# Optimization experiments

Measured on AMD Instinct MI355X. Metric: run time of the kernel, lower is better.

The kernel has to match this reference:

```python
import jax, jax.numpy as jnp
import numpy as np


def setup_inputs() -> dict:
    key = jax.random.key(0)
    ks = jax.random.split(key, 6)
    N, E, D = 50000, 400000, 128
    x = jax.random.normal(ks[0], (N, D), dtype=jnp.float32)
    edge_attr = jax.random.normal(ks[1], (E, D), dtype=jnp.float32)
    edge_index = jax.random.randint(ks[2], (2, E), 0, N, dtype=jnp.int64)
    # LatentMLP: two linear layers (3*D -> D -> D) with ReLU activations
    W1 = jax.random.normal(ks[3], (3 * D, D), dtype=jnp.float32) * (1.0 / np.sqrt(3 * D))
    b1 = jnp.zeros((D,), dtype=jnp.float32)
    W2 = jax.random.normal(ks[4], (D, D), dtype=jnp.float32) * (1.0 / np.sqrt(D))
    b2 = jnp.zeros((D,), dtype=jnp.float32)
    return {"x": x, "edge_attr": edge_attr, "edge_index": edge_index,
            "W1": W1, "b1": b1, "W2": W2, "b2": b2}


def reference(x, edge_attr, edge_index, W1, b1, W2, b2):
    src, dst = edge_index[0], edge_index[1]
    # gather node features per edge: [E, D] each
    agg = jnp.concatenate([x[src], x[dst], edge_attr], axis=1)  # [E, 3D]
    h = jax.nn.relu(agg @ W1 + b1)   # [E, D]
    out = jax.nn.relu(h @ W2 + b2)   # [E, D] -> new edge_attr
    return out
```

## Files before the change

kernel.cpp:

```cpp
#include <hip/hip_runtime.h>
#include <hip/hip_bf16.h>

typedef __bf16 bf16_t;
typedef __bf16 bf16x8 __attribute__((ext_vector_type(8)));
typedef __bf16 bf16x4 __attribute__((ext_vector_type(4)));
typedef float  f32x4  __attribute__((ext_vector_type(4)));

#define D  128
#define BM 128

__device__ __forceinline__ int swz(int r, int c) {
    return (r * D + c) ^ ((r & 7) << 3);
}

__global__ void prep_weights_kernel(const float* __restrict__ W1,
                                    const float* __restrict__ W2,
                                    bf16_t* __restrict__ ws) {
    int t = blockIdx.x * 256 + threadIdx.x;
    int s = t >> 14, r = t & 16383;
    int n = r >> 7, k = r & 127;
    float v = (s < 3) ? W1[(s * 128 + k) * 128 + n] : W2[k * 128 + n];
    ws[t] = (bf16_t)v;
}

__global__ __launch_bounds__(256, 2)
void fused_edge_mlp_kernel(const float* __restrict__ x,
                           const float* __restrict__ ea,
                           const int* __restrict__ ei,
                           const bf16_t* __restrict__ ws,
                           const float* __restrict__ b1,
                           const float* __restrict__ b2,
                           float* __restrict__ out,
                           int E) {
    __shared__ __align__(16) bf16_t Ab[BM * D];
    __shared__ __align__(16) bf16_t Bb[D * D];

    const int tid  = threadIdx.x;
    const int lane = tid & 63;
    const int wv   = tid >> 6;
    const int col0 = lane & 15;
    const int krow = lane >> 4;
    const int l31  = lane & 31;
    const int half = lane >> 5;
    const int e0   = blockIdx.x * BM;

    const int erL  = min(e0 + wv * 32 + l31, E - 1);
    const int sidx = ei[erL];
    const int didx = ei[E + erL];

    const int brow_t = tid >> 4;
    const int bslot  = (tid & 15) * 8;

    f32x4  abuf[16];
    bf16x8 bnext[8];

    {
        const bf16_t* base = ws;
#pragma unroll
        for (int j = 0; j < 8; j++)
            bnext[j] = *(const bf16x8*)(base + (j * 16 + brow_t) * 128 + bslot);
    }
#pragma unroll
    for (int j = 0; j < 16; j++) {
        int r = j * 2 + half;
        int g = __shfl(sidx, r);
        abuf[j] = *(const f32x4*)(x + (long long)g * D + l31 * 4);
    }

    float bias1[8], bias2[8];
#pragma unroll
    for (int n = 0; n < 8; n++) { bias1[n] = b1[n*16 + col0]; bias2[n] = b2[n*16 + col0]; }

#pragma unroll
    for (int j = 0; j < 8; j++)
        *(bf16x8*)&Bb[swz(j * 16 + brow_t, bslot)] = bnext[j];
#pragma unroll
    for (int j = 0; j < 16; j++) {
        int r = j * 2 + half;
        f32x4 v = abuf[j];
        bf16x4 hv = { (bf16_t)v.x, (bf16_t)v.y, (bf16_t)v.z, (bf16_t)v.w };
        *(bf16x4*)&Ab[swz(wv * 32 + r, l31 * 4)] = hv;
    }
    __syncthreads();

    f32x4 acc[2][8];
#pragma unroll
    for (int m = 0; m < 2; m++)
#pragma unroll
        for (int n = 0; n < 8; n++) acc[m][n] = (f32x4){0.f, 0.f, 0.f, 0.f};

#pragma unroll
    for (int p = 0; p < 4; p++) {
        if (p < 3) {
            const bf16_t* base = ws + (p + 1) * 16384;
#pragma unroll
            for (int j = 0; j < 8; j++)
                bnext[j] = *(const bf16x8*)(base + (j * 16 + brow_t) * 128 + bslot);
        }
        if (p < 2) {
#pragma unroll
            for (int j = 0; j < 16; j++) {
                int r = j * 2 + half;
                const float* rp;
                if (p == 0) { int g = __shfl(didx, r); rp = x + (long long)g * D; }
                else        { int e = min(e0 + wv * 32 + r, E - 1); rp = ea + (long long)e * D; }
                abuf[j] = *(const f32x4*)(rp + l31 * 4);
            }
        }

#pragma unroll
        for (int kk = 0; kk < 4; kk++) {
            bf16x8 a0 = *(const bf16x8*)&Ab[swz(wv*32 +      col0, kk*32 + krow*8)];
            bf16x8 a1 = *(const bf16x8*)&Ab[swz(wv*32 + 16 + col0, kk*32 + krow*8)];
#pragma unroll
            for (int n = 0; n < 8; n++) {
                bf16x8 b = *(const bf16x8*)&Bb[swz(n*16 + col0, kk*32 + krow*8)];
                acc[0][n] = __builtin_amdgcn_mfma_f32_16x16x32_bf16(a0, b, acc[0][n], 0, 0, 0);
                acc[1][n] = __builtin_amdgcn_mfma_f32_16x16x32_bf16(a1, b, acc[1][n], 0, 0, 0);
            }
        }

        if (p < 2) {
#pragma unroll
            for (int j = 0; j < 16; j++) {
                int r = j * 2 + half;
                f32x4 v = abuf[j];
                bf16x4 hv = { (bf16_t)v.x, (bf16_t)v.y, (bf16_t)v.z, (bf16_t)v.w };
                *(bf16x4*)&Ab[swz(wv * 32 + r, l31 * 4)] = hv;
            }
        }
        if (p == 2) {
#pragma unroll
            for (int m = 0; m < 2; m++)
#pragma unroll
                for (int n = 0; n < 8; n++)
#pragma unroll
                    for (int ri = 0; ri < 4; ri++) {
                        float hv = fmaxf(acc[m][n][ri] + bias1[n], 0.f);
                        Ab[swz(wv*32 + m*16 + krow*4 + ri, n*16 + col0)] = (bf16_t)hv;
                    }
#pragma unroll
            for (int m = 0; m < 2; m++)
#pragma unroll
                for (int n = 0; n < 8; n++) acc[m][n] = (f32x4){0.f, 0.f, 0.f, 0.f};
        }
        if (p < 3) {
            __syncthreads();
#pragma unroll
            for (int j = 0; j < 8; j++)
                *(bf16x8*)&Bb[swz(j * 16 + brow_t, bslot)] = bnext[j];
            __syncthreads();
        }
    }

#pragma unroll
    for (int m = 0; m < 2; m++)
#pragma unroll
        for (int n = 0; n < 8; n++)
#pragma unroll
            for (int ri = 0; ri < 4; ri++) {
                int row = wv*32 + m*16 + krow*4 + ri;
                int e = e0 + row;
                if (e < E) out[(long long)e * D + n*16 + col0] = fmaxf(acc[m][n][ri] + bias2[n], 0.f);
            }
}

extern "C" void kernel_launch(void* const* d_in, const int* in_sizes, int n_in,
                              void* d_out, int out_size, void* d_ws, size_t ws_size,
                              hipStream_t stream) {
    const float* x  = (const float*)d_in[0];
    const float* ea = (const float*)d_in[1];
    const int*   ei = (const int*)d_in[2];
    const float* W1 = (const float*)d_in[3];
    const float* b1 = (const float*)d_in[4];
    const float* W2 = (const float*)d_in[5];
    const float* b2 = (const float*)d_in[6];
    float* out = (float*)d_out;

    const int E = in_sizes[1] / D;

    bf16_t* wsl = (bf16_t*)d_ws;

    prep_weights_kernel<<<256, 256, 0, stream>>>(W1, W2, wsl);

    int nblocks = (E + BM - 1) / BM;
    fused_edge_mlp_kernel<<<nblocks, 256, 0, stream>>>(x, ea, ei, wsl, b1, b2, out, E);
}
```

Before: 144.2 us.

## Read pre-swizzled MFMA weight fragments from global instead of staging in LDS

The weight prep kernel now writes W1 and W2 in the exact per-lane bf16x8 fragment order that the MFMA B operand expects. The main kernel loads B fragments straight from global memory (served by L1/L2) rather than staging each 128x128 weight slice in shared memory. This drops the 32KB B buffer and every block-wide __syncthreads, and raises the launch-bounds occupancy hint from 2 to 3 blocks per CU. In exchange, each wave re-reads the full weight set through the cache hierarchy with no register prefetch, which adds L2 traffic and exposes load latency right before the MFMAs in a kernel that is already bandwidth-heavy.

```diff
diff --git a/kernel.cpp b/kernel.cpp
--- a/kernel.cpp
+++ b/kernel.cpp
@@ -17,13 +17,21 @@
                                     const float* __restrict__ W2,
                                     bf16_t* __restrict__ ws) {
     int t = blockIdx.x * 256 + threadIdx.x;
-    int s = t >> 14, r = t & 16383;
-    int n = r >> 7, k = r & 127;
-    float v = (s < 3) ? W1[(s * 128 + k) * 128 + n] : W2[k * 128 + n];
-    ws[t] = (bf16_t)v;
+    int lane = t & 63, g = t >> 6;
+    int n = g & 7, kk = (g >> 3) & 3, s = g >> 5;
+    int row = n * 16 + (lane & 15);
+    int k0 = kk * 32 + (lane >> 4) * 8;
+    bf16x8 v;
+#pragma unroll
+    for (int j = 0; j < 8; j++) {
+        int k = k0 + j;
+        float f = (s < 3) ? W1[(s * 128 + k) * 128 + row] : W2[k * 128 + row];
+        v[j] = (bf16_t)f;
+    }
+    *(bf16x8*)(ws + t * 8) = v;
 }
 
-__global__ __launch_bounds__(256, 2)
+__global__ __launch_bounds__(256, 3)
 void fused_edge_mlp_kernel(const float* __restrict__ x,
                            const float* __restrict__ ea,
                            const int* __restrict__ ei,
@@ -33,7 +41,6 @@
                            float* __restrict__ out,
                            int E) {
     __shared__ __align__(16) bf16_t Ab[BM * D];
-    __shared__ __align__(16) bf16_t Bb[D * D];
 
     const int tid  = threadIdx.x;
     const int lane = tid & 63;
@@ -48,32 +55,17 @@
     const int sidx = ei[erL];
     const int didx = ei[E + erL];
 
-    const int brow_t = tid >> 4;
-    const int bslot  = (tid & 15) * 8;
+    f32x4 abuf[16];
 
-    f32x4  abuf[16];
-    bf16x8 bnext[8];
-
-    {
-        const bf16_t* base = ws;
-#pragma unroll
-        for (int j = 0; j < 8; j++)
-            bnext[j] = *(const bf16x8*)(base + (j * 16 + brow_t) * 128 + bslot);
-    }
 #pragma unroll
     for (int j = 0; j < 16; j++) {
         int r = j * 2 + half;
         int g = __shfl(sidx, r);
         abuf[j] = *(const f32x4*)(x + (long long)g * D + l31 * 4);
     }
-
     float bias1[8], bias2[8];
 #pragma unroll
     for (int n = 0; n < 8; n++) { bias1[n] = b1[n*16 + col0]; bias2[n] = b2[n*16 + col0]; }
-
-#pragma unroll
-    for (int j = 0; j < 8; j++)
-        *(bf16x8*)&Bb[swz(j * 16 + brow_t, bslot)] = bnext[j];
 #pragma unroll
     for (int j = 0; j < 16; j++) {
         int r = j * 2 + half;
@@ -81,7 +73,6 @@
         bf16x4 hv = { (bf16_t)v.x, (bf16_t)v.y, (bf16_t)v.z, (bf16_t)v.w };
         *(bf16x4*)&Ab[swz(wv * 32 + r, l31 * 4)] = hv;
     }
-    __syncthreads();
 
     f32x4 acc[2][8];
 #pragma unroll
@@ -91,12 +82,6 @@
 
 #pragma unroll
     for (int p = 0; p < 4; p++) {
-        if (p < 3) {
-            const bf16_t* base = ws + (p + 1) * 16384;
-#pragma unroll
-            for (int j = 0; j < 8; j++)
-                bnext[j] = *(const bf16x8*)(base + (j * 16 + brow_t) * 128 + bslot);
-        }
         if (p < 2) {
 #pragma unroll
             for (int j = 0; j < 16; j++) {
@@ -112,9 +97,10 @@
         for (int kk = 0; kk < 4; kk++) {
             bf16x8 a0 = *(const bf16x8*)&Ab[swz(wv*32 +      col0, kk*32 + krow*8)];
             bf16x8 a1 = *(const bf16x8*)&Ab[swz(wv*32 + 16 + col0, kk*32 + krow*8)];
+            const bf16_t* bbase = ws + ((p * 4 + kk) * 8 * 64 + lane) * 8;
 #pragma unroll
             for (int n = 0; n < 8; n++) {
-                bf16x8 b = *(const bf16x8*)&Bb[swz(n*16 + col0, kk*32 + krow*8)];
+                bf16x8 b = *(const bf16x8*)(bbase + n * 512);
                 acc[0][n] = __builtin_amdgcn_mfma_f32_16x16x32_bf16(a0, b, acc[0][n], 0, 0, 0);
                 acc[1][n] = __builtin_amdgcn_mfma_f32_16x16x32_bf16(a1, b, acc[1][n], 0, 0, 0);
             }
@@ -143,13 +129,6 @@
             for (int m = 0; m < 2; m++)
 #pragma unroll
                 for (int n = 0; n < 8; n++) acc[m][n] = (f32x4){0.f, 0.f, 0.f, 0.f};
-        }
-        if (p < 3) {
-            __syncthreads();
-#pragma unroll
-            for (int j = 0; j < 8; j++)
-                *(bf16x8*)&Bb[swz(j * 16 + brow_t, bslot)] = bnext[j];
-            __syncthreads();
         }
     }
 
@@ -181,7 +160,7 @@
 
     bf16_t* wsl = (bf16_t*)d_ws;
 
-    prep_weights_kernel<<<256, 256, 0, stream>>>(W1, W2, wsl);
+    prep_weights_kernel<<<32, 256, 0, stream>>>(W1, W2, wsl);
 
     int nblocks = (E + BM - 1) / BM;
     fused_edge_mlp_kernel<<<nblocks, 256, 0, stream>>>(x, ea, ei, wsl, b1, b2, out, E);
```

Measured after the change: 190.9 us. 1.32x slower.

## Load gathered A operands directly into MFMA registers and halve edge tile

Applied to the files above, without the earlier changes.

Each lane now loads its gathered x/edge_attr rows straight from global memory in the MFMA A-fragment layout, converts them to bf16 in registers, and skips the LDS staging of the A tile. Only the hidden activation h goes through shared memory. The edge tile shrinks from 128 to 64 rows, each wave holds one 16-row fragment, and launch bounds go to 3 blocks per CU, aiming to cut LDS traffic and raise occupancy. In exchange, each B tile loaded into LDS is reused by half as many rows, so there are more blocks, more weight reloads per edge and more syncs per edge. Global loads are also less coalesced, each lane reading 32-byte pieces of rows.

```diff
diff --git a/kernel.cpp b/kernel.cpp
--- a/kernel.cpp
+++ b/kernel.cpp
@@ -3,11 +3,10 @@
 
 typedef __bf16 bf16_t;
 typedef __bf16 bf16x8 __attribute__((ext_vector_type(8)));
-typedef __bf16 bf16x4 __attribute__((ext_vector_type(4)));
 typedef float  f32x4  __attribute__((ext_vector_type(4)));
 
 #define D  128
-#define BM 128
+#define BM 64
 
 __device__ __forceinline__ int swz(int r, int c) {
     return (r * D + c) ^ ((r & 7) << 3);
@@ -23,7 +22,7 @@
     ws[t] = (bf16_t)v;
 }
 
-__global__ __launch_bounds__(256, 2)
+__global__ __launch_bounds__(256, 3)
 void fused_edge_mlp_kernel(const float* __restrict__ x,
                            const float* __restrict__ ea,
                            const int* __restrict__ ei,
@@ -32,26 +31,24 @@
                            const float* __restrict__ b2,
                            float* __restrict__ out,
                            int E) {
-    __shared__ __align__(16) bf16_t Ab[BM * D];
     __shared__ __align__(16) bf16_t Bb[D * D];
+    __shared__ __align__(16) bf16_t Hb[BM * D];
 
     const int tid  = threadIdx.x;
     const int lane = tid & 63;
     const int wv   = tid >> 6;
     const int col0 = lane & 15;
     const int krow = lane >> 4;
-    const int l31  = lane & 31;
-    const int half = lane >> 5;
     const int e0   = blockIdx.x * BM;
 
-    const int erL  = min(e0 + wv * 32 + l31, E - 1);
+    const int erL  = min(e0 + wv * 16 + col0, E - 1);
     const int sidx = ei[erL];
     const int didx = ei[E + erL];
 
     const int brow_t = tid >> 4;
     const int bslot  = (tid & 15) * 8;
 
-    f32x4  abuf[16];
+    f32x4  afA[8];
     bf16x8 bnext[8];
 
     {
@@ -60,13 +57,14 @@
         for (int j = 0; j < 8; j++)
             bnext[j] = *(const bf16x8*)(base + (j * 16 + brow_t) * 128 + bslot);
     }
+    {
+        const float* rp = x + (long long)sidx * D + krow * 8;
 #pragma unroll
-    for (int j = 0; j < 16; j++) {
-        int r = j * 2 + half;
-        int g = __shfl(sidx, r);
-        abuf[j] = *(const f32x4*)(x + (long long)g * D + l31 * 4);
+        for (int kk = 0; kk < 4; kk++) {
+            afA[kk*2]   = *(const f32x4*)(rp + kk*32);
+            afA[kk*2+1] = *(const f32x4*)(rp + kk*32 + 4);
+        }
     }
-
     float bias1[8], bias2[8];
 #pragma unroll
     for (int n = 0; n < 8; n++) { bias1[n] = b1[n*16 + col0]; bias2[n] = b2[n*16 + col0]; }
@@ -74,20 +72,12 @@
 #pragma unroll
     for (int j = 0; j < 8; j++)
         *(bf16x8*)&Bb[swz(j * 16 + brow_t, bslot)] = bnext[j];
+
+    f32x4 acc[8];
 #pragma unroll
-    for (int j = 0; j < 16; j++) {
-        int r = j * 2 + half;
-        f32x4 v = abuf[j];
-        bf16x4 hv = { (bf16_t)v.x, (bf16_t)v.y, (bf16_t)v.z, (bf16_t)v.w };
-        *(bf16x4*)&Ab[swz(wv * 32 + r, l31 * 4)] = hv;
-    }
+    for (int n = 0; n < 8; n++) acc[n] = (f32x4){0.f, 0.f, 0.f, 0.f};
+
     __syncthreads();
-
-    f32x4 acc[2][8];
-#pragma unroll
-    for (int m = 0; m < 2; m++)
-#pragma unroll
-        for (int n = 0; n < 8; n++) acc[m][n] = (f32x4){0.f, 0.f, 0.f, 0.f};
 
 #pragma unroll
     for (int p = 0; p < 4; p++) {
@@ -97,53 +87,50 @@
             for (int j = 0; j < 8; j++)
                 bnext[j] = *(const bf16x8*)(base + (j * 16 + brow_t) * 128 + bslot);
         }
+
+        bf16x8 a_cur[4];
+        if (p < 3) {
+#pragma unroll
+            for (int kk = 0; kk < 4; kk++) {
+                f32x4 lo = afA[kk*2], hi = afA[kk*2+1];
+                a_cur[kk] = (bf16x8){ (bf16_t)lo.x,(bf16_t)lo.y,(bf16_t)lo.z,(bf16_t)lo.w,
+                                      (bf16_t)hi.x,(bf16_t)hi.y,(bf16_t)hi.z,(bf16_t)hi.w };
+            }
+        }
         if (p < 2) {
+            const float* rp = (p == 0) ? (x + (long long)didx * D + krow * 8)
+                                       : (ea + (long long)erL * D + krow * 8);
 #pragma unroll
-            for (int j = 0; j < 16; j++) {
-                int r = j * 2 + half;
-                const float* rp;
-                if (p == 0) { int g = __shfl(didx, r); rp = x + (long long)g * D; }
-                else        { int e = min(e0 + wv * 32 + r, E - 1); rp = ea + (long long)e * D; }
-                abuf[j] = *(const f32x4*)(rp + l31 * 4);
+            for (int kk = 0; kk < 4; kk++) {
+                afA[kk*2]   = *(const f32x4*)(rp + kk*32);
+                afA[kk*2+1] = *(const f32x4*)(rp + kk*32 + 4);
             }
         }
 
 #pragma unroll
         for (int kk = 0; kk < 4; kk++) {
-            bf16x8 a0 = *(const bf16x8*)&Ab[swz(wv*32 +      col0, kk*32 + krow*8)];
-            bf16x8 a1 = *(const bf16x8*)&Ab[swz(wv*32 + 16 + col0, kk*32 + krow*8)];
+            bf16x8 a;
+            if (p < 3) a = a_cur[kk];
+            else       a = *(const bf16x8*)&Hb[swz(wv*16 + col0, kk*32 + krow*8)];
 #pragma unroll
             for (int n = 0; n < 8; n++) {
                 bf16x8 b = *(const bf16x8*)&Bb[swz(n*16 + col0, kk*32 + krow*8)];
-                acc[0][n] = __builtin_amdgcn_mfma_f32_16x16x32_bf16(a0, b, acc[0][n], 0, 0, 0);
-                acc[1][n] = __builtin_amdgcn_mfma_f32_16x16x32_bf16(a1, b, acc[1][n], 0, 0, 0);
+                acc[n] = __builtin_amdgcn_mfma_f32_16x16x32_bf16(a, b, acc[n], 0, 0, 0);
             }
         }
 
-        if (p < 2) {
-#pragma unroll
-            for (int j = 0; j < 16; j++) {
-                int r = j * 2 + half;
-                f32x4 v = abuf[j];
-                bf16x4 hv = { (bf16_t)v.x, (bf16_t)v.y, (bf16_t)v.z, (bf16_t)v.w };
-                *(bf16x4*)&Ab[swz(wv * 32 + r, l31 * 4)] = hv;
-            }
-        }
         if (p == 2) {
 #pragma unroll
-            for (int m = 0; m < 2; m++)
+            for (int n = 0; n < 8; n++)
 #pragma unroll
-                for (int n = 0; n < 8; n++)
+                for (int ri = 0; ri < 4; ri++) {
+                    float hv = fmaxf(acc[n][ri] + bias1[n], 0.f);
+                    Hb[swz(wv*16 + krow*4 + ri, n*16 + col0)] = (bf16_t)hv;
+                }
 #pragma unroll
-                    for (int ri = 0; ri < 4; ri++) {
-                        float hv = fmaxf(acc[m][n][ri] + bias1[n], 0.f);
-                        Ab[swz(wv*32 + m*16 + krow*4 + ri, n*16 + col0)] = (bf16_t)hv;
-                    }
-#pragma unroll
-            for (int m = 0; m < 2; m++)
-#pragma unroll
-                for (int n = 0; n < 8; n++) acc[m][n] = (f32x4){0.f, 0.f, 0.f, 0.f};
+            for (int n = 0; n < 8; n++) acc[n] = (f32x4){0.f, 0.f, 0.f, 0.f};
         }
+
         if (p < 3) {
             __syncthreads();
 #pragma unroll
@@ -154,15 +141,13 @@
     }
 
 #pragma unroll
-    for (int m = 0; m < 2; m++)
+    for (int n = 0; n < 8; n++)
 #pragma unroll
-        for (int n = 0; n < 8; n++)
-#pragma unroll
-            for (int ri = 0; ri < 4; ri++) {
-                int row = wv*32 + m*16 + krow*4 + ri;
-                int e = e0 + row;
-                if (e < E) out[(long long)e * D + n*16 + col0] = fmaxf(acc[m][n][ri] + bias2[n], 0.f);
-            }
+        for (int ri = 0; ri < 4; ri++) {
+            int row = wv*16 + krow*4 + ri;
+            int e = e0 + row;
+            if (e < E) out[(long long)e * D + n*16 + col0] = fmaxf(acc[n][ri] + bias2[n], 0.f);
+        }
 }
 
 extern "C" void kernel_launch(void* const* d_in, const int* in_sizes, int n_in,
```

Result: slower. 169.6 us (+17.6%).

## Pre-convert node features to bf16 and gather both endpoints upfront

Applied to the files above, without the earlier changes.

A prep kernel now converts the whole node feature matrix x to bf16 in the workspace, alongside the weight transpose. The fused kernel gathers src and dst rows as bf16 at the start, halving gather bytes and removing per-edge conversion, and only the edge_attr stream is loaded in the pipeline. This costs an extra full pass over x (read fp32, write bf16) plus more registers held for both gathered buffers. The prep kernel hardcodes 3125 x-blocks, which matches N*D/2048 only for this input size.

```diff
diff --git a/kernel.cpp b/kernel.cpp
--- a/kernel.cpp
+++ b/kernel.cpp
@@ -13,18 +13,30 @@
     return (r * D + c) ^ ((r & 7) << 3);
 }
 
-__global__ void prep_weights_kernel(const float* __restrict__ W1,
-                                    const float* __restrict__ W2,
-                                    bf16_t* __restrict__ ws) {
-    int t = blockIdx.x * 256 + threadIdx.x;
-    int s = t >> 14, r = t & 16383;
-    int n = r >> 7, k = r & 127;
-    float v = (s < 3) ? W1[(s * 128 + k) * 128 + n] : W2[k * 128 + n];
-    ws[t] = (bf16_t)v;
+__global__ void prep_kernel(const float* __restrict__ W1,
+                            const float* __restrict__ W2,
+                            const float* __restrict__ x,
+                            bf16_t* __restrict__ ws,
+                            bf16_t* __restrict__ xh) {
+    int b = blockIdx.x;
+    if (b < 3125) {
+        int t = b * 256 + threadIdx.x;
+        f32x4 lo = *(const f32x4*)(x + t * 8);
+        f32x4 hi = *(const f32x4*)(x + t * 8 + 4);
+        bf16x8 v = { (bf16_t)lo.x,(bf16_t)lo.y,(bf16_t)lo.z,(bf16_t)lo.w,
+                     (bf16_t)hi.x,(bf16_t)hi.y,(bf16_t)hi.z,(bf16_t)hi.w };
+        *(bf16x8*)(xh + t * 8) = v;
+    } else {
+        int t = (b - 3125) * 256 + threadIdx.x;
+        int s = t >> 14, r = t & 16383;
+        int n = r >> 7, k = r & 127;
+        float v = (s < 3) ? W1[(s * 128 + k) * 128 + n] : W2[k * 128 + n];
+        ws[t] = (bf16_t)v;
+    }
 }
 
 __global__ __launch_bounds__(256, 2)
-void fused_edge_mlp_kernel(const float* __restrict__ x,
+void fused_edge_mlp_kernel(const bf16_t* __restrict__ xh,
                            const float* __restrict__ ea,
                            const int* __restrict__ ei,
                            const bf16_t* __restrict__ ws,
@@ -43,75 +55,73 @@
     const int l31  = lane & 31;
     const int half = lane >> 5;
     const int e0   = blockIdx.x * BM;
-
-    const int erL  = min(e0 + wv * 32 + l31, E - 1);
-    const int sidx = ei[erL];
-    const int didx = ei[E + erL];
+    const int r0   = wv * 32;
+
+    const int erI  = min(e0 + r0 + l31, E - 1);
+    const int sidx = ei[erI];
+    const int didx = ei[E + erI];
+
+    const int gr = lane >> 4;
+    const int gc = (lane & 15) * 8;
 
     const int brow_t = tid >> 4;
     const int bslot  = (tid & 15) * 8;
 
-    f32x4  abuf[16];
-    bf16x8 bnext[8];
-
-    {
-        const bf16_t* base = ws;
-#pragma unroll
-        for (int j = 0; j < 8; j++)
-            bnext[j] = *(const bf16x8*)(base + (j * 16 + brow_t) * 128 + bslot);
-    }
-#pragma unroll
-    for (int j = 0; j < 16; j++) {
-        int r = j * 2 + half;
-        int g = __shfl(sidx, r);
-        abuf[j] = *(const f32x4*)(x + (long long)g * D + l31 * 4);
-    }
-
+    bf16x8 bufS[8], bufD[8], bnext[8];
+    f32x4  eabuf[16];
+
+#pragma unroll
+    for (int j = 0; j < 8; j++)
+        bnext[j] = *(const bf16x8*)(ws + (j * 16 + brow_t) * 128 + bslot);
+#pragma unroll
+    for (int j = 0; j < 8; j++) {
+        int g = __shfl(sidx, j * 4 + gr);
+        bufS[j] = *(const bf16x8*)(xh + g * D + gc);
+    }
+#pragma unroll
+    for (int j = 0; j < 8; j++) {
+        int g = __shfl(didx, j * 4 + gr);
+        bufD[j] = *(const bf16x8*)(xh + g * D + gc);
+    }
     float bias1[8], bias2[8];
 #pragma unroll
     for (int n = 0; n < 8; n++) { bias1[n] = b1[n*16 + col0]; bias2[n] = b2[n*16 + col0]; }
 
+#pragma unroll
+    for (int j = 0; j < 8; j++)
+        *(bf16x8*)&Ab[swz(r0 + j * 4 + gr, gc)] = bufS[j];
 #pragma unroll
     for (int j = 0; j < 8; j++)
         *(bf16x8*)&Bb[swz(j * 16 + brow_t, bslot)] = bnext[j];
-#pragma unroll
-    for (int j = 0; j < 16; j++) {
-        int r = j * 2 + half;
-        f32x4 v = abuf[j];
-        bf16x4 hv = { (bf16_t)v.x, (bf16_t)v.y, (bf16_t)v.z, (bf16_t)v.w };
-        *(bf16x4*)&Ab[swz(wv * 32 + r, l31 * 4)] = hv;
-    }
+
+    f32x4 acc[2][8];
+#pragma unroll
+    for (int m = 0; m < 2; m++)
+#pragma unroll
+        for (int n = 0; n < 8; n++) acc[m][n] = (f32x4){0.f, 0.f, 0.f, 0.f};
+
     __syncthreads();
 
-    f32x4 acc[2][8];
-#pragma unroll
-    for (int m = 0; m < 2; m++)
-#pragma unroll
-        for (int n = 0; n < 8; n++) acc[m][n] = (f32x4){0.f, 0.f, 0.f, 0.f};
-
-#pragma unroll
-    for (int p = 0; p < 4; p++) {
-        if (p < 3) {
-            const bf16_t* base = ws + (p + 1) * 16384;
+#pragma unroll
+    for (int q = 0; q < 4; q++) {
+        if (q < 3) {
+            const bf16_t* base = ws + (q + 1) * 16384;
 #pragma unroll
             for (int j = 0; j < 8; j++)
                 bnext[j] = *(const bf16x8*)(base + (j * 16 + brow_t) * 128 + bslot);
         }
-        if (p < 2) {
+        if (q == 0) {
 #pragma unroll
             for (int j = 0; j < 16; j++) {
-                int r = j * 2 + half;
-                const float* rp;
-                if (p == 0) { int g = __shfl(didx, r); rp = x + (long long)g * D; }
-                else        { int e = min(e0 + wv * 32 + r, E - 1); rp = ea + (long long)e * D; }
-                abuf[j] = *(const f32x4*)(rp + l31 * 4);
+                int e = min(e0 + r0 + j * 2 + half, E - 1);
+                eabuf[j] = *(const f32x4*)(ea + e * D + l31 * 4);
             }
         }
 
 #pragma unroll
         for (int kk = 0; kk < 4; kk++) {
-            bf16x8 a0 = *(const bf16x8*)&Ab[swz(wv*32 +      col0, kk*32 + krow*8)];
-            bf16x8 a1 = *(const bf16x8*)&Ab[swz(wv*32 + 16 + col0, kk*32 + krow*8)];
+            bf16x8 a0 = *(const bf16x8*)&Ab[swz(r0 +      col0, kk*32 + krow*8)];
+            bf16x8 a1 = *(const bf16x8*)&Ab[swz(r0 + 16 + col0, kk*32 + krow*8)];
 #pragma unroll
             for (int n = 0; n < 8; n++) {
                 bf16x8 b = *(const bf16x8*)&Bb[swz(n*16 + col0, kk*32 + krow*8)];
@@ -120,16 +130,18 @@
             }
         }
 
-        if (p < 2) {
+        if (q == 0) {
+#pragma unroll
+            for (int j = 0; j < 8; j++)
+                *(bf16x8*)&Ab[swz(r0 + j * 4 + gr, gc)] = bufD[j];
+        } else if (q == 1) {
 #pragma unroll
             for (int j = 0; j < 16; j++) {
-                int r = j * 2 + half;
-                f32x4 v = abuf[j];
+                f32x4 v = eabuf[j];
                 bf16x4 hv = { (bf16_t)v.x, (bf16_t)v.y, (bf16_t)v.z, (bf16_t)v.w };
-                *(bf16x4*)&Ab[swz(wv * 32 + r, l31 * 4)] = hv;
-            }
-        }
-        if (p == 2) {
+                *(bf16x4*)&Ab[swz(r0 + j * 2 + half, l31 * 4)] = hv;
+            }
+        } else if (q == 2) {
 #pragma unroll
             for (int m = 0; m < 2; m++)
 #pragma unroll
@@ -137,14 +149,15 @@
 #pragma unroll
                     for (int ri = 0; ri < 4; ri++) {
                         float hv = fmaxf(acc[m][n][ri] + bias1[n], 0.f);
-                        Ab[swz(wv*32 + m*16 + krow*4 + ri, n*16 + col0)] = (bf16_t)hv;
+                        Ab[swz(r0 + m*16 + krow*4 + ri, n*16 + col0)] = (bf16_t)hv;
                     }
 #pragma unroll
             for (int m = 0; m < 2; m++)
 #pragma unroll
                 for (int n = 0; n < 8; n++) acc[m][n] = (f32x4){0.f, 0.f, 0.f, 0.f};
         }
-        if (p < 3) {
+
+        if (q < 3) {
             __syncthreads();
 #pragma unroll
             for (int j = 0; j < 8; j++)
@@ -159,9 +172,8 @@
         for (int n = 0; n < 8; n++)
 #pragma unroll
             for (int ri = 0; ri < 4; ri++) {
-                int row = wv*32 + m*16 + krow*4 + ri;
-                int e = e0 + row;
-                if (e < E) out[(long long)e * D + n*16 + col0] = fmaxf(acc[m][n][ri] + bias2[n], 0.f);
+                int e = e0 + r0 + m*16 + krow*4 + ri;
+                if (e < E) out[e * D + n*16 + col0] = fmaxf(acc[m][n][ri] + bias2[n], 0.f);
             }
 }
 
@@ -178,11 +190,14 @@
     float* out = (float*)d_out;
 
     const int E = in_sizes[1] / D;
+    const int N = in_sizes[0] / D;
 
     bf16_t* wsl = (bf16_t*)d_ws;
-
-    prep_weights_kernel<<<256, 256, 0, stream>>>(W1, W2, wsl);
+    bf16_t* xh  = (bf16_t*)d_ws + 4 * 16384;
+
+    const int xblocks = (N * D) / (256 * 8);
+    prep_kernel<<<xblocks + 256, 256, 0, stream>>>(W1, W2, x, wsl, xh);
 
     int nblocks = (E + BM - 1) / BM;
-    fused_edge_mlp_kernel<<<nblocks, 256, 0, stream>>>(x, ea, ei, wsl, b1, b2, out, E);
-}
+    fused_edge_mlp_kernel<<<nblocks, 256, 0, stream>>>(xh, ea, ei, wsl, b1, b2, out, E);
+}
```

Result: slower. 153.0 us (+6.1%).
